# Optimization experiments

Measured on AMD Instinct MI355X. Metric: run time of the kernel, lower is better.

Reference implementation:

```python
import jax, jax.numpy as jnp
import numpy as np

K_HOPS = 3
NUM_GRAPHS = 64
GN_EPS = 1e-5


def setup_inputs() -> dict:
    key = jax.random.key(0)
    ks = jax.random.split(key, 6)
    N, E, F = 50000, 625000, 128
    y = jax.random.normal(ks[0], (N, F), dtype=jnp.float32)
    edge_index = jax.random.randint(ks[1], (2, E), 0, N, dtype=jnp.int64)
    edge_weight = jax.random.uniform(ks[2], (E,), dtype=jnp.float32)
    batch = jnp.sort(jax.random.randint(ks[3], (N,), 0, NUM_GRAPHS, dtype=jnp.int64))
    tag_w = jax.random.normal(ks[4], (K_HOPS + 1, F, F), dtype=jnp.float32) * (1.0 / np.sqrt(F))
    tag_b = jnp.zeros((F,), dtype=jnp.float32)
    gn_weight = jnp.ones((F,), dtype=jnp.float32)
    gn_bias = jnp.zeros((F,), dtype=jnp.float32)
    gn_mean_scale = jnp.ones((F,), dtype=jnp.float32)
    return {"y": y, "edge_index": edge_index, "edge_weight": edge_weight,
            "batch": batch, "tag_w": tag_w, "tag_b": tag_b,
            "gn_weight": gn_weight, "gn_bias": gn_bias, "gn_mean_scale": gn_mean_scale}


def reference(y, edge_index, edge_weight, batch, tag_w, tag_b, gn_weight, gn_bias, gn_mean_scale):
    N = y.shape[0]
    src, dst = edge_index[0], edge_index[1]

    # --- TAGConv: symmetric gcn_norm (no self-loops), K hops ---
    deg = jax.ops.segment_sum(edge_weight, dst, num_segments=N)  # [N]
    dinv = jnp.where(deg > 0, jax.lax.rsqrt(jnp.maximum(deg, 1e-30)), 0.0)
    norm = dinv[src] * edge_weight * dinv[dst]  # [E]

    h = y
    out = h @ tag_w[0]
    for k in range(1, K_HOPS + 1):
        # one hop of message passing: gather from src, scatter-sum at dst
        h = jax.ops.segment_sum(norm[:, None] * h[src], dst, num_segments=N)  # [N,F]
        out = out + h @ tag_w[k]
    out = out + tag_b

    # --- GraphNorm over per-graph segments ---
    cnt = jax.ops.segment_sum(jnp.ones((N,), out.dtype), batch, num_segments=NUM_GRAPHS)
    cnt = jnp.maximum(cnt, 1.0)[:, None]  # [G,1]
    mean = jax.ops.segment_sum(out, batch, num_segments=NUM_GRAPHS) / cnt  # [G,F]
    xc = out - gn_mean_scale * mean[batch]
    var = jax.ops.segment_sum(xc * xc, batch, num_segments=NUM_GRAPHS) / cnt  # [G,F]
    hn = gn_weight * xc * jax.lax.rsqrt(var[batch] + GN_EPS) + gn_bias

    # --- activation; dropout is identity in eval mode; residual ---
    h_act = jax.nn.relu(hn)
    return y + h_act
```

## Files before the change

kernel.cpp:

```cpp
#include <hip/hip_runtime.h>

#define F 128
#define GRAPHS 64
#define GN_EPS 1e-5f
#define SCAN_B 256
#define PB 256

typedef short short8 __attribute__((ext_vector_type(8)));
typedef float f32x4 __attribute__((ext_vector_type(4)));

__device__ __forceinline__ unsigned short f2b(float f) {
    unsigned u = __float_as_uint(f);
    unsigned r = (u + 0x7fffu + ((u >> 16) & 1u)) >> 16;
    return (unsigned short)r;
}
__device__ __forceinline__ float b2f(unsigned short h) {
    return __uint_as_float(((unsigned)h) << 16);
}

__global__ __launch_bounds__(256) void prep_kernel(const int* __restrict__ ei,
                            int* __restrict__ hist_t, int E, int NB, int chunk,
                            const float4* __restrict__ y, ushort4* __restrict__ hs0,
                            int n4, int fbl,
                            const float* __restrict__ tw, unsigned short* __restrict__ wf,
                            const int* __restrict__ batch, int* __restrict__ gstart, int n) {
    int b = blockIdx.x;
    if (b < PB) {
        __shared__ int hist[256];
        hist[threadIdx.x] = 0;
        __syncthreads();
        int e0 = b * chunk, e1 = min(e0 + chunk, E);
        for (int e = e0 + threadIdx.x; e < e1; e += 256)
            atomicAdd(&hist[ei[E + e] >> 8], 1);
        __syncthreads();
        for (int k = threadIdx.x; k < NB; k += 256)
            hist_t[k * PB + b] = hist[k];
    } else if (b < PB + fbl) {
        int i = (b - PB) * 256 + threadIdx.x;
        if (i < n4) {
            float4 v = y[i];
            hs0[i] = make_ushort4(f2b(v.x), f2b(v.y), f2b(v.z), f2b(v.w));
        }
    } else if (b < PB + fbl + 256) {
        int i = (b - PB - fbl) * 256 + threadIdx.x;
        int seg = i >> 14;
        int r = i & 16383;
        int kb = r >> 12;
        int wc = (r >> 11) & 1;
        int nt = (r >> 9) & 3;
        int lane = (r >> 3) & 63;
        int j = i & 7;
        int k = kb * 32 + (lane >> 4) * 8 + j;
        int nn = wc * 64 + nt * 16 + (lane & 15);
        wf[i] = f2b(tw[seg * 16384 + k * 128 + nn]);
    } else {
        int i = (b - PB - fbl - 256) * 256 + threadIdx.x;
        if (i < n) {
            int bb = batch[i];
            if (i == 0) {
                for (int g = 0; g <= bb; ++g) gstart[g] = 0;
            } else {
                int bp = batch[i - 1];
                for (int g = bp + 1; g <= bb; ++g) gstart[g] = i;
            }
            if (i == n - 1) {
                for (int g = bb + 1; g <= GRAPHS; ++g) gstart[g] = n;
            }
        }
    }
}

__global__ void scanA_kernel(const int* __restrict__ in, int* __restrict__ ex,
                             int* __restrict__ blockSums, int n) {
    __shared__ int s[SCAN_B];
    int i = blockIdx.x * SCAN_B + threadIdx.x;
    int v = (i < n) ? in[i] : 0;
    s[threadIdx.x] = v;
    __syncthreads();
    for (int off = 1; off < SCAN_B; off <<= 1) {
        int t = (threadIdx.x >= off) ? s[threadIdx.x - off] : 0;
        __syncthreads();
        s[threadIdx.x] += t;
        __syncthreads();
    }
    if (i < n) ex[i] = s[threadIdx.x] - v;
    if (threadIdx.x == SCAN_B - 1) blockSums[blockIdx.x] = s[SCAN_B - 1];
}

__global__ void scanB_kernel(int* __restrict__ ex, const int* __restrict__ blockSums,
                             int n, int nb) {
    __shared__ int s[SCAN_B];
    int t = threadIdx.x;
    int v = (t < nb) ? blockSums[t] : 0;
    s[t] = v;
    __syncthreads();
    for (int off = 1; off < SCAN_B; off <<= 1) {
        int x = (t >= off) ? s[t - off] : 0;
        __syncthreads();
        s[t] += x;
        __syncthreads();
    }
    int pre = (blockIdx.x == 0) ? 0 : s[blockIdx.x - 1];
    int i = blockIdx.x * SCAN_B + t;
    if (i < n) ex[i] += pre;
}

__global__ __launch_bounds__(256) void part_kernel(const int* __restrict__ ei,
                                                   const float* __restrict__ ew,
                                                   const int* __restrict__ ex,
                                                   uint2* __restrict__ part,
                                                   int E, int NB, int chunk) {
    __shared__ int cur[256];
    int k = blockIdx.x;
    for (int b = threadIdx.x; b < NB; b += 256) cur[b] = ex[b * PB + k];
    __syncthreads();
    int e0 = k * chunk, e1 = min(e0 + chunk, E);
    for (int e = e0 + threadIdx.x; e < e1; e += 256) {
        int dst = ei[E + e];
        int src = ei[e];
        float w = ew[e];
        int slot = atomicAdd(&cur[dst >> 8], 1);
        part[slot] = make_uint2(((unsigned)dst << 16) | (unsigned)src, __float_as_uint(w));
    }
}

__global__ __launch_bounds__(256) void bucket_kernel(const uint2* __restrict__ part,
                                                     const int* __restrict__ ex,
                                                     float* __restrict__ dinv,
                                                     int* __restrict__ offs,
                                                     unsigned* __restrict__ csr,
                                                     int N, int NB, int E) {
    __shared__ float degf[256];
    __shared__ int cnte[256];
    __shared__ int scn[256];
    __shared__ int cur2[256];
    int b = blockIdx.x, t = threadIdx.x;
    degf[t] = 0.f;
    cnte[t] = 0;
    __syncthreads();
    int s0 = ex[b * PB];
    int s1 = (b + 1 < NB) ? ex[(b + 1) * PB] : E;
    for (int i = s0 + t; i < s1; i += 256) {
        uint2 p = part[i];
        int dl = (p.x >> 16) & 255;
        atomicAdd(&degf[dl], __uint_as_float(p.y));
        atomicAdd(&cnte[dl], 1);
    }
    __syncthreads();
    int v = cnte[t];
    scn[t] = v;
    __syncthreads();
    for (int off = 1; off < 256; off <<= 1) {
        int x = (t >= off) ? scn[t - off] : 0;
        __syncthreads();
        scn[t] += x;
        __syncthreads();
    }
    int node = b * 256 + t;
    int base = s0 + scn[t] - v;
    if (node < N) {
        float d = degf[t];
        dinv[node] = (d > 0.f) ? rsqrtf(fmaxf(d, 1e-30f)) : 0.f;
        offs[node] = base;
    }
    if (b == 0 && t == 0) offs[N] = E;
    cur2[t] = base;
    __syncthreads();
    for (int i = s0 + t; i < s1; i += 256) {
        uint2 p = part[i];
        int dl = (p.x >> 16) & 255;
        unsigned src = p.x & 0xffffu;
        int slot = atomicAdd(&cur2[dl], 1);
        csr[slot] = (src << 16) | (unsigned)f2b(__uint_as_float(p.y));
    }
}

__global__ void wfix_kernel(unsigned* __restrict__ csr, const float* __restrict__ dinv, int E) {
    int i = blockIdx.x * 256 + threadIdx.x;
    if (i >= E) return;
    unsigned v = csr[i];
    unsigned src = v >> 16;
    float w = b2f((unsigned short)(v & 0xffffu)) * dinv[src];
    csr[i] = (src << 16) | (unsigned)f2b(w);
}

__global__ __launch_bounds__(256) void hop_kernel(const unsigned short* __restrict__ hin,
                                                  unsigned short* __restrict__ hout,
                                                  const int* __restrict__ offs,
                                                  const unsigned* __restrict__ csr,
                                                  const float* __restrict__ dinv, int n) {
    int lane = threadIdx.x & 63;
    int node = blockIdx.x * 4 + (threadIdx.x >> 6);
    if (node >= n) return;
    int g = lane >> 4, fl = lane & 15;
    int e0 = offs[node], e1 = offs[node + 1];
    float acc[8] = {};
    for (int j = e0; j < e1; j += 16) {
        int base = j + g * 4;
        int c0 = min(base + 0, e1 - 1), c1 = min(base + 1, e1 - 1);
        int c2 = min(base + 2, e1 - 1), c3 = min(base + 3, e1 - 1);
        unsigned ed0 = csr[c0], ed1 = csr[c1], ed2 = csr[c2], ed3 = csr[c3];
        float w0 = (base + 0 < e1) ? b2f((unsigned short)(ed0 & 0xffffu)) : 0.f;
        float w1 = (base + 1 < e1) ? b2f((unsigned short)(ed1 & 0xffffu)) : 0.f;
        float w2 = (base + 2 < e1) ? b2f((unsigned short)(ed2 & 0xffffu)) : 0.f;
        float w3 = (base + 3 < e1) ? b2f((unsigned short)(ed3 & 0xffffu)) : 0.f;
        short8 h0 = *(const short8*)(hin + (size_t)(ed0 >> 16) * 128 + fl * 8);
        short8 h1 = *(const short8*)(hin + (size_t)(ed1 >> 16) * 128 + fl * 8);
        short8 h2 = *(const short8*)(hin + (size_t)(ed2 >> 16) * 128 + fl * 8);
        short8 h3 = *(const short8*)(hin + (size_t)(ed3 >> 16) * 128 + fl * 8);
        #pragma unroll
        for (int k = 0; k < 8; ++k) {
            acc[k] += w0 * b2f((unsigned short)h0[k]) + w1 * b2f((unsigned short)h1[k]);
            acc[k] += w2 * b2f((unsigned short)h2[k]) + w3 * b2f((unsigned short)h3[k]);
        }
    }
    #pragma unroll
    for (int k = 0; k < 8; ++k) {
        acc[k] += __shfl_xor(acc[k], 16);
        acc[k] += __shfl_xor(acc[k], 32);
    }
    if (lane < 16) {
        float dd = dinv[node];
        short8 o;
        #pragma unroll
        for (int k = 0; k < 8; ++k) o[k] = (short)f2b(acc[k] * dd);
        *(short8*)(hout + (size_t)node * 128 + fl * 8) = o;
    }
}

__global__ __launch_bounds__(256) void gemm_kernel(const unsigned short* __restrict__ hcat,
                                                   const unsigned short* __restrict__ Wf,
                                                   const float* __restrict__ bias,
                                                   unsigned short* __restrict__ outb,
                                                   int M, size_t NF) {
    __shared__ unsigned short As[4][4096];
    int lane = threadIdx.x & 63;
    int wid = threadIdx.x >> 6;
    int wr = wid & 1, wc = wid >> 1;
    int quad = lane >> 4, l15 = lane & 15;
    int row0 = blockIdx.x * 64;
    unsigned short* myA = As[wid];
    f32x4 acc[2][4] = {};

    for (int s = 0; s < 4; ++s) {
        const unsigned short* Aseg = hcat + (size_t)s * NF;
        short8 stg[8];
        #pragma unroll
        for (int i = 0; i < 8; ++i) {
            int flat = i * 64 + lane;
            int r = flat >> 4, c = flat & 15;
            stg[i] = *(const short8*)(Aseg + (size_t)(row0 + wr * 32 + r) * 128 + c * 8);
        }
        #pragma unroll
        for (int i = 0; i < 8; ++i) {
            int flat = i * 64 + lane;
            int r = flat >> 4, c = flat & 15;
            *(short8*)&myA[(r * 16 + (c ^ (r & 15))) * 8] = stg[i];
        }
        #pragma unroll
        for (int kb = 0; kb < 4; ++kb) {
            int swz = ((kb * 4 + quad) ^ l15) * 8;
            short8 a0 = *(short8*)&myA[l15 * 128 + swz];
            short8 a1 = *(short8*)&myA[(16 + l15) * 128 + swz];
            const unsigned short* bb = Wf + (size_t)(((s * 4 + kb) * 2 + wc) * 4) * 512 + lane * 8;
            short8 b0 = *(const short8*)(bb + 0 * 512);
            short8 b1 = *(const short8*)(bb + 1 * 512);
            short8 b2 = *(const short8*)(bb + 2 * 512);
            short8 b3 = *(const short8*)(bb + 3 * 512);
            acc[0][0] = __builtin_amdgcn_mfma_f32_16x16x32_bf16(a0, b0, acc[0][0], 0, 0, 0);
            acc[0][1] = __builtin_amdgcn_mfma_f32_16x16x32_bf16(a0, b1, acc[0][1], 0, 0, 0);
            acc[0][2] = __builtin_amdgcn_mfma_f32_16x16x32_bf16(a0, b2, acc[0][2], 0, 0, 0);
            acc[0][3] = __builtin_amdgcn_mfma_f32_16x16x32_bf16(a0, b3, acc[0][3], 0, 0, 0);
            acc[1][0] = __builtin_amdgcn_mfma_f32_16x16x32_bf16(a1, b0, acc[1][0], 0, 0, 0);
            acc[1][1] = __builtin_amdgcn_mfma_f32_16x16x32_bf16(a1, b1, acc[1][1], 0, 0, 0);
            acc[1][2] = __builtin_amdgcn_mfma_f32_16x16x32_bf16(a1, b2, acc[1][2], 0, 0, 0);
            acc[1][3] = __builtin_amdgcn_mfma_f32_16x16x32_bf16(a1, b3, acc[1][3], 0, 0, 0);
        }
    }

    #pragma unroll
    for (int mt = 0; mt < 2; ++mt) {
        #pragma unroll
        for (int r = 0; r < 4; ++r) {
            int row = row0 + wr * 32 + mt * 16 + quad * 4 + r;
            if (row < M) {
                #pragma unroll
                for (int nt = 0; nt < 4; ++nt) {
                    int col = wc * 64 + nt * 16 + l15;
                    outb[(size_t)row * 128 + col] = f2b(acc[mt][nt][r] + bias[col]);
                }
            }
        }
    }
}

#define STAT_NODES 32
__global__ __launch_bounds__(256) void stats_kernel(const unsigned* __restrict__ ob2,
                                                    const int* __restrict__ batch,
                                                    float* __restrict__ S1, float* __restrict__ S2,
                                                    int n) {
    int fp = threadIdx.x & 63;
    int par = threadIdx.x >> 6;
    int base = blockIdx.x * STAT_NODES;
    int n1 = min(base + STAT_NODES, n);
    int i0 = base + par;
    if (i0 >= n1) return;
    float s1a = 0.f, s2a = 0.f, s1b = 0.f, s2b = 0.f;
    int curg = batch[i0];
    for (int i = i0; i < n1; i += 4) {
        int g = batch[i];
        if (g != curg) {
            atomicAdd(&S1[curg * F + fp * 2 + 0], s1a);
            atomicAdd(&S2[curg * F + fp * 2 + 0], s2a);
            atomicAdd(&S1[curg * F + fp * 2 + 1], s1b);
            atomicAdd(&S2[curg * F + fp * 2 + 1], s2b);
            s1a = s2a = s1b = s2b = 0.f; curg = g;
        }
        unsigned v2 = ob2[(size_t)i * 64 + fp];
        float va = b2f((unsigned short)(v2 & 0xffffu));
        float vb = b2f((unsigned short)(v2 >> 16));
        s1a += va; s2a += va * va;
        s1b += vb; s2b += vb * vb;
    }
    atomicAdd(&S1[curg * F + fp * 2 + 0], s1a);
    atomicAdd(&S2[curg * F + fp * 2 + 0], s2a);
    atomicAdd(&S1[curg * F + fp * 2 + 1], s1b);
    atomicAdd(&S2[curg * F + fp * 2 + 1], s2b);
}

__global__ void final_kernel(const ushort4* __restrict__ yb, const ushort4* __restrict__ ob,
                             const int* __restrict__ batch, const float* __restrict__ S1,
                             const float* __restrict__ S2, const int* __restrict__ gstart,
                             const float* __restrict__ gnw, const float* __restrict__ gnb,
                             const float* __restrict__ gms,
                             float4* __restrict__ res, int n) {
    int idx = blockIdx.x * blockDim.x + threadIdx.x;
    if (idx >= n * 32) return;
    int node = idx >> 5;
    int q = idx & 31;
    int g = batch[node];
    float rc = 1.f / fmaxf((float)(gstart[g + 1] - gstart[g]), 1.f);
    int base = g * 128 + q * 4;
    float4 s1 = *(const float4*)&S1[base];
    float4 s2 = *(const float4*)&S2[base];
    float4 w  = *(const float4*)&gnw[q * 4];
    float4 bb = *(const float4*)&gnb[q * 4];
    float4 sc = *(const float4*)&gms[q * 4];
    ushort4 yv = yb[idx];
    ushort4 ov = ob[idx];
    float4 r;
    {
        float m = s1.x * rc, e2 = s2.x * rc, s = sc.x;
        float var = e2 - (2.f * s - s * s) * m * m;
        float A = w.x * rsqrtf(var + GN_EPS);
        r.x = b2f(yv.x) + fmaxf(0.f, (b2f(ov.x) - s * m) * A + bb.x);
    }
    {
        float m = s1.y * rc, e2 = s2.y * rc, s = sc.y;
        float var = e2 - (2.f * s - s * s) * m * m;
        float A = w.y * rsqrtf(var + GN_EPS);
        r.y = b2f(yv.y) + fmaxf(0.f, (b2f(ov.y) - s * m) * A + bb.y);
    }
    {
        float m = s1.z * rc, e2 = s2.z * rc, s = sc.z;
        float var = e2 - (2.f * s - s * s) * m * m;
        float A = w.z * rsqrtf(var + GN_EPS);
        r.z = b2f(yv.z) + fmaxf(0.f, (b2f(ov.z) - s * m) * A + bb.z);
    }
    {
        float m = s1.w * rc, e2 = s2.w * rc, s = sc.w;
        float var = e2 - (2.f * s - s * s) * m * m;
        float A = w.w * rsqrtf(var + GN_EPS);
        r.w = b2f(yv.w) + fmaxf(0.f, (b2f(ov.w) - s * m) * A + bb.w);
    }
    res[idx] = r;
}

extern "C" void kernel_launch(void* const* d_in, const int* in_sizes, int n_in,
                              void* d_out, int out_size, void* d_ws, size_t ws_size,
                              hipStream_t stream) {
    const float* y     = (const float*)d_in[0];
    const int*   ei    = (const int*)d_in[1];
    const float* ew    = (const float*)d_in[2];
    const int*   batch = (const int*)d_in[3];
    const float* tag_w = (const float*)d_in[4];
    const float* tag_b = (const float*)d_in[5];
    const float* gnw   = (const float*)d_in[6];
    const float* gnb   = (const float*)d_in[7];
    const float* gms   = (const float*)d_in[8];
    float* res = (float*)d_out;

    const int N = in_sizes[0] / F;
    const int E = in_sizes[1] / 2;
    const size_t NF = (size_t)N * F;
    const int NB = (N + 255) >> 8;
    const int NH = NB * PB;
    const int chunk = (E + PB - 1) / PB;

    char* p = (char*)d_ws;
    float* S1 = (float*)p;       p += (size_t)GRAPHS * F * 4;
    float* S2 = (float*)p;       p += (size_t)GRAPHS * F * 4;
    size_t zeroBytes = (size_t)(p - (char*)d_ws);
    int*   gstart = (int*)p;     p += 512;
    float* dinv = (float*)p;     p += (size_t)N * 4;
    int*   offs = (int*)p;       p += (size_t)(N + 4) * 4;
    int*   hist_t = (int*)p;     p += (size_t)NH * 4;
    int*   ex = (int*)p;         p += (size_t)(NH + 4) * 4;
    int*   blockSums = (int*)p;  p += 4096;
    uint2* part = (uint2*)p;     p += (size_t)E * 8;
    unsigned* csr = (unsigned*)p; p += (size_t)E * 4;
    unsigned short* Wf = (unsigned short*)p; p += 4 * 128 * 128 * 2;
    unsigned short* hcat = (unsigned short*)p; p += NF * 2 * 4;
    unsigned short* outb = (unsigned short*)p; p += NF * 2;
    p += 4096;

    hipMemsetAsync(d_ws, 0, zeroBytes, stream);

    int n4 = N * 32;
    int fb = (n4 + 255) / 256;
    int gb = (N + 255) / 256;
    int hsb = (NH + SCAN_B - 1) / SCAN_B;

    unsigned short* hs0 = hcat;
    unsigned short* hs1 = hcat + NF;
    unsigned short* hs2 = hcat + 2 * NF;
    unsigned short* hs3 = hcat + 3 * NF;

    prep_kernel<<<PB + fb + 256 + gb, 256, 0, stream>>>(ei, hist_t, E, NB, chunk,
                                                        (const float4*)y, (ushort4*)hs0, n4, fb,
                                                        tag_w, Wf, batch, gstart, N);
    scanA_kernel<<<hsb, SCAN_B, 0, stream>>>(hist_t, ex, blockSums, NH);
    scanB_kernel<<<hsb, SCAN_B, 0, stream>>>(ex, blockSums, NH, hsb);
    part_kernel<<<PB, 256, 0, stream>>>(ei, ew, ex, part, E, NB, chunk);
    bucket_kernel<<<NB, 256, 0, stream>>>(part, ex, dinv, offs, csr, N, NB, E);
    wfix_kernel<<<(E + 255) / 256, 256, 0, stream>>>(csr, dinv, E);

    int hb = (N + 3) / 4;
    hop_kernel<<<hb, 256, 0, stream>>>(hs0, hs1, offs, csr, dinv, N);
    hop_kernel<<<hb, 256, 0, stream>>>(hs1, hs2, offs, csr, dinv, N);
    hop_kernel<<<hb, 256, 0, stream>>>(hs2, hs3, offs, csr, dinv, N);

    gemm_kernel<<<(N + 63) / 64, 256, 0, stream>>>(hcat, Wf, tag_b, outb, N, NF);

    stats_kernel<<<(N + STAT_NODES - 1) / STAT_NODES, 256, 0, stream>>>((const unsigned*)outb,
                                                                        batch, S1, S2, N);

    final_kernel<<<(N * 32 + 255) / 256, 256, 0, stream>>>((const ushort4*)hs0, (const ushort4*)outb,
                                                           batch, S1, S2, gstart, gnw, gnb, gms,
                                                           (float4*)res, N);
}
```

Measured before the change: 246.8 us.

## Fuse all stages into one cooperative persistent kernel with grid syncs

Replaces the dozen separate launches (memset, prep, two scans, partition, bucket, weight-fix, three hops, gemm, stats, final) with a single cooperative mega-kernel that loops over tasks and separates phases with grid-wide syncs. The global scan is folded into the partition phase, where each block recomputes its prefix from the histogram. The weight-fix pass is folded into the first hop, and stats is merged into the gemm phase. This removes per-launch overhead and intermediate passes, but limits parallelism to resident blocks and adds grid-sync cost. A multi-kernel fallback is kept for devices without cooperative launch.

```diff
diff --git a/kernel.cpp b/kernel.cpp
--- a/kernel.cpp
+++ b/kernel.cpp
@@ -1,9 +1,11 @@
 #include <hip/hip_runtime.h>
+#include <hip/hip_cooperative_groups.h>
+
+namespace cg = cooperative_groups;
 
 #define F 128
 #define GRAPHS 64
 #define GN_EPS 1e-5f
-#define SCAN_B 256
 #define PB 256
 
 typedef short short8 __attribute__((ext_vector_type(8)));
@@ -18,363 +20,417 @@
     return __uint_as_float(((unsigned)h) << 16);
 }
 
-__global__ __launch_bounds__(256) void prep_kernel(const int* __restrict__ ei,
-                            int* __restrict__ hist_t, int E, int NB, int chunk,
-                            const float4* __restrict__ y, ushort4* __restrict__ hs0,
-                            int n4, int fbl,
-                            const float* __restrict__ tw, unsigned short* __restrict__ wf,
-                            const int* __restrict__ batch, int* __restrict__ gstart, int n) {
-    int b = blockIdx.x;
-    if (b < PB) {
-        __shared__ int hist[256];
-        hist[threadIdx.x] = 0;
-        __syncthreads();
-        int e0 = b * chunk, e1 = min(e0 + chunk, E);
-        for (int e = e0 + threadIdx.x; e < e1; e += 256)
-            atomicAdd(&hist[ei[E + e] >> 8], 1);
-        __syncthreads();
-        for (int k = threadIdx.x; k < NB; k += 256)
-            hist_t[k * PB + b] = hist[k];
-    } else if (b < PB + fbl) {
-        int i = (b - PB) * 256 + threadIdx.x;
-        if (i < n4) {
-            float4 v = y[i];
-            hs0[i] = make_ushort4(f2b(v.x), f2b(v.y), f2b(v.z), f2b(v.w));
-        }
-    } else if (b < PB + fbl + 256) {
-        int i = (b - PB - fbl) * 256 + threadIdx.x;
-        int seg = i >> 14;
-        int r = i & 16383;
-        int kb = r >> 12;
-        int wc = (r >> 11) & 1;
-        int nt = (r >> 9) & 3;
-        int lane = (r >> 3) & 63;
-        int j = i & 7;
-        int k = kb * 32 + (lane >> 4) * 8 + j;
-        int nn = wc * 64 + nt * 16 + (lane & 15);
-        wf[i] = f2b(tw[seg * 16384 + k * 128 + nn]);
-    } else {
-        int i = (b - PB - fbl - 256) * 256 + threadIdx.x;
-        if (i < n) {
-            int bb = batch[i];
-            if (i == 0) {
-                for (int g = 0; g <= bb; ++g) gstart[g] = 0;
-            } else {
-                int bp = batch[i - 1];
-                for (int g = bp + 1; g <= bb; ++g) gstart[g] = i;
-            }
-            if (i == n - 1) {
-                for (int g = bb + 1; g <= GRAPHS; ++g) gstart[g] = n;
-            }
-        }
-    }
-}
-
-__global__ void scanA_kernel(const int* __restrict__ in, int* __restrict__ ex,
-                             int* __restrict__ blockSums, int n) {
-    __shared__ int s[SCAN_B];
-    int i = blockIdx.x * SCAN_B + threadIdx.x;
-    int v = (i < n) ? in[i] : 0;
-    s[threadIdx.x] = v;
-    __syncthreads();
-    for (int off = 1; off < SCAN_B; off <<= 1) {
-        int t = (threadIdx.x >= off) ? s[threadIdx.x - off] : 0;
-        __syncthreads();
-        s[threadIdx.x] += t;
-        __syncthreads();
-    }
-    if (i < n) ex[i] = s[threadIdx.x] - v;
-    if (threadIdx.x == SCAN_B - 1) blockSums[blockIdx.x] = s[SCAN_B - 1];
-}
-
-__global__ void scanB_kernel(int* __restrict__ ex, const int* __restrict__ blockSums,
-                             int n, int nb) {
-    __shared__ int s[SCAN_B];
+struct MArgs {
+    const float* y; const int* ei; const float* ew; const int* batch;
+    const float* tw; const float* tb; const float* gnw; const float* gnb; const float* gms;
+    float* res;
+    float* S1; float* S2; int* gstart; float* dinv; int* offs; int* hist_t; int* bbase;
+    uint2* part; unsigned* csr; unsigned short* Wf; unsigned short* hcat; unsigned short* outb;
+    int N, E, NB, chunk, fb, gb;
+    size_t NF;
+};
+
+__device__ void ph_prep(const MArgs& a, char* smem) {
+    int* hist = (int*)smem;
+    const int t0 = 256;
+    const int t1 = t0 + a.fb;
+    const int t2 = t1 + 256;
+    const int t3 = t2 + a.gb;
+    const int t4 = t3 + 8;
+    int tid = threadIdx.x;
+    for (int task = blockIdx.x; task < t4; task += gridDim.x) {
+        if (task < t0) {
+            __syncthreads();
+            hist[tid] = 0;
+            __syncthreads();
+            int e0 = task * a.chunk, e1 = min(e0 + a.chunk, a.E);
+            for (int e = e0 + tid; e < e1; e += 256)
+                atomicAdd(&hist[a.ei[a.E + e] >> 8], 1);
+            __syncthreads();
+            for (int k = tid; k < a.NB; k += 256)
+                a.hist_t[k * PB + task] = hist[k];
+        } else if (task < t1) {
+            int i = (task - t0) * 256 + tid;
+            if (i < a.N * 32) {
+                float4 v = ((const float4*)a.y)[i];
+                ((ushort4*)a.hcat)[i] = make_ushort4(f2b(v.x), f2b(v.y), f2b(v.z), f2b(v.w));
+            }
+        } else if (task < t2) {
+            int i = (task - t1) * 256 + tid;
+            int seg = i >> 14;
+            int r = i & 16383;
+            int kb = r >> 12;
+            int wcc = (r >> 11) & 1;
+            int ntt = (r >> 9) & 3;
+            int lane = (r >> 3) & 63;
+            int j = i & 7;
+            int k = kb * 32 + (lane >> 4) * 8 + j;
+            int nn = wcc * 64 + ntt * 16 + (lane & 15);
+            a.Wf[i] = f2b(a.tw[seg * 16384 + k * 128 + nn]);
+        } else if (task < t3) {
+            int i = (task - t2) * 256 + tid;
+            if (i < a.N) {
+                int bb = a.batch[i];
+                if (i == 0) {
+                    for (int g = 0; g <= bb; ++g) a.gstart[g] = 0;
+                } else {
+                    int bp = a.batch[i - 1];
+                    for (int g = bp + 1; g <= bb; ++g) a.gstart[g] = i;
+                }
+                if (i == a.N - 1) {
+                    for (int g = bb + 1; g <= GRAPHS; ++g) a.gstart[g] = a.N;
+                }
+            }
+        } else {
+            int z = task - t3;
+            float* dst = a.S1 + z * 2048;
+            for (int i2 = tid; i2 < 2048; i2 += 256) dst[i2] = 0.f;
+        }
+    }
+}
+
+__device__ void ph_part(const MArgs& a, char* smem) {
+    int* cur = (int*)smem;
+    int* rs  = cur + 256;
     int t = threadIdx.x;
-    int v = (t < nb) ? blockSums[t] : 0;
-    s[t] = v;
-    __syncthreads();
-    for (int off = 1; off < SCAN_B; off <<= 1) {
-        int x = (t >= off) ? s[t - off] : 0;
-        __syncthreads();
-        s[t] += x;
-        __syncthreads();
-    }
-    int pre = (blockIdx.x == 0) ? 0 : s[blockIdx.x - 1];
-    int i = blockIdx.x * SCAN_B + t;
-    if (i < n) ex[i] += pre;
-}
-
-__global__ __launch_bounds__(256) void part_kernel(const int* __restrict__ ei,
-                                                   const float* __restrict__ ew,
-                                                   const int* __restrict__ ex,
-                                                   uint2* __restrict__ part,
-                                                   int E, int NB, int chunk) {
-    __shared__ int cur[256];
-    int k = blockIdx.x;
-    for (int b = threadIdx.x; b < NB; b += 256) cur[b] = ex[b * PB + k];
-    __syncthreads();
-    int e0 = k * chunk, e1 = min(e0 + chunk, E);
-    for (int e = e0 + threadIdx.x; e < e1; e += 256) {
-        int dst = ei[E + e];
-        int src = ei[e];
-        float w = ew[e];
-        int slot = atomicAdd(&cur[dst >> 8], 1);
-        part[slot] = make_uint2(((unsigned)dst << 16) | (unsigned)src, __float_as_uint(w));
-    }
-}
-
-__global__ __launch_bounds__(256) void bucket_kernel(const uint2* __restrict__ part,
-                                                     const int* __restrict__ ex,
-                                                     float* __restrict__ dinv,
-                                                     int* __restrict__ offs,
-                                                     unsigned* __restrict__ csr,
-                                                     int N, int NB, int E) {
-    __shared__ float degf[256];
-    __shared__ int cnte[256];
-    __shared__ int scn[256];
-    __shared__ int cur2[256];
-    int b = blockIdx.x, t = threadIdx.x;
-    degf[t] = 0.f;
-    cnte[t] = 0;
-    __syncthreads();
-    int s0 = ex[b * PB];
-    int s1 = (b + 1 < NB) ? ex[(b + 1) * PB] : E;
-    for (int i = s0 + t; i < s1; i += 256) {
-        uint2 p = part[i];
-        int dl = (p.x >> 16) & 255;
-        atomicAdd(&degf[dl], __uint_as_float(p.y));
-        atomicAdd(&cnte[dl], 1);
-    }
-    __syncthreads();
-    int v = cnte[t];
-    scn[t] = v;
-    __syncthreads();
-    for (int off = 1; off < 256; off <<= 1) {
-        int x = (t >= off) ? scn[t - off] : 0;
-        __syncthreads();
-        scn[t] += x;
-        __syncthreads();
-    }
-    int node = b * 256 + t;
-    int base = s0 + scn[t] - v;
-    if (node < N) {
-        float d = degf[t];
-        dinv[node] = (d > 0.f) ? rsqrtf(fmaxf(d, 1e-30f)) : 0.f;
-        offs[node] = base;
-    }
-    if (b == 0 && t == 0) offs[N] = E;
-    cur2[t] = base;
-    __syncthreads();
-    for (int i = s0 + t; i < s1; i += 256) {
-        uint2 p = part[i];
-        int dl = (p.x >> 16) & 255;
-        unsigned src = p.x & 0xffffu;
-        int slot = atomicAdd(&cur2[dl], 1);
-        csr[slot] = (src << 16) | (unsigned)f2b(__uint_as_float(p.y));
-    }
-}
-
-__global__ void wfix_kernel(unsigned* __restrict__ csr, const float* __restrict__ dinv, int E) {
-    int i = blockIdx.x * 256 + threadIdx.x;
-    if (i >= E) return;
-    unsigned v = csr[i];
-    unsigned src = v >> 16;
-    float w = b2f((unsigned short)(v & 0xffffu)) * dinv[src];
-    csr[i] = (src << 16) | (unsigned)f2b(w);
-}
-
-__global__ __launch_bounds__(256) void hop_kernel(const unsigned short* __restrict__ hin,
-                                                  unsigned short* __restrict__ hout,
-                                                  const int* __restrict__ offs,
-                                                  const unsigned* __restrict__ csr,
-                                                  const float* __restrict__ dinv, int n) {
+    for (int k = blockIdx.x; k < PB; k += gridDim.x) {
+        __syncthreads();
+        int total = 0, pref = 0;
+        if (t < a.NB) {
+            const int4* row = (const int4*)(a.hist_t + t * PB);
+            for (int q = 0; q < PB / 4; ++q) {
+                int4 v = row[q];
+                int c4 = q * 4;
+                total += v.x + v.y + v.z + v.w;
+                if (c4 + 4 <= k) pref += v.x + v.y + v.z + v.w;
+                else {
+                    if (c4 + 0 < k) pref += v.x;
+                    if (c4 + 1 < k) pref += v.y;
+                    if (c4 + 2 < k) pref += v.z;
+                    if (c4 + 3 < k) pref += v.w;
+                }
+            }
+        }
+        rs[t] = (t < a.NB) ? total : 0;
+        __syncthreads();
+        for (int off = 1; off < 256; off <<= 1) {
+            int x = (t >= off) ? rs[t - off] : 0;
+            __syncthreads();
+            rs[t] += x;
+            __syncthreads();
+        }
+        int rowStart = (t > 0) ? rs[t - 1] : 0;
+        cur[t] = rowStart + pref;
+        if (k == 0 && t <= a.NB) a.bbase[t] = rowStart;
+        __syncthreads();
+        int e0 = k * a.chunk, e1 = min(e0 + a.chunk, a.E);
+        for (int e = e0 + t; e < e1; e += 256) {
+            int dst = a.ei[a.E + e];
+            int src = a.ei[e];
+            float w = a.ew[e];
+            int slot = atomicAdd(&cur[dst >> 8], 1);
+            a.part[slot] = make_uint2(((unsigned)dst << 16) | (unsigned)src, __float_as_uint(w));
+        }
+    }
+}
+
+__device__ void ph_bucket(const MArgs& a, char* smem) {
+    float* degf = (float*)smem;
+    int* cnte = (int*)(smem + 1024);
+    int* scn  = (int*)(smem + 2048);
+    int* cur2 = (int*)(smem + 3072);
+    int t = threadIdx.x;
+    for (int b = blockIdx.x; b < a.NB; b += gridDim.x) {
+        __syncthreads();
+        degf[t] = 0.f;
+        cnte[t] = 0;
+        __syncthreads();
+        int s0 = a.bbase[b];
+        int s1 = a.bbase[b + 1];
+        for (int i = s0 + t; i < s1; i += 256) {
+            uint2 pp = a.part[i];
+            int dl = (pp.x >> 16) & 255;
+            atomicAdd(&degf[dl], __uint_as_float(pp.y));
+            atomicAdd(&cnte[dl], 1);
+        }
+        __syncthreads();
+        int v = cnte[t];
+        scn[t] = v;
+        __syncthreads();
+        for (int off = 1; off < 256; off <<= 1) {
+            int x = (t >= off) ? scn[t - off] : 0;
+            __syncthreads();
+            scn[t] += x;
+            __syncthreads();
+        }
+        int node = b * 256 + t;
+        int base = s0 + scn[t] - v;
+        if (node < a.N) {
+            float d = degf[t];
+            a.dinv[node] = (d > 0.f) ? rsqrtf(fmaxf(d, 1e-30f)) : 0.f;
+            a.offs[node] = base;
+        }
+        if (b == 0 && t == 0) a.offs[a.N] = a.E;
+        cur2[t] = base;
+        __syncthreads();
+        for (int i = s0 + t; i < s1; i += 256) {
+            uint2 pp = a.part[i];
+            int dl = (pp.x >> 16) & 255;
+            unsigned src = pp.x & 0xffffu;
+            int slot = atomicAdd(&cur2[dl], 1);
+            a.csr[slot] = (src << 16) | (unsigned)f2b(__uint_as_float(pp.y));
+        }
+    }
+}
+
+template<bool FIX>
+__device__ void ph_hop(const MArgs& a, const unsigned short* __restrict__ hin,
+                       unsigned short* __restrict__ hout) {
     int lane = threadIdx.x & 63;
-    int node = blockIdx.x * 4 + (threadIdx.x >> 6);
-    if (node >= n) return;
-    int g = lane >> 4, fl = lane & 15;
-    int e0 = offs[node], e1 = offs[node + 1];
-    float acc[8] = {};
-    for (int j = e0; j < e1; j += 16) {
-        int base = j + g * 4;
-        int c0 = min(base + 0, e1 - 1), c1 = min(base + 1, e1 - 1);
-        int c2 = min(base + 2, e1 - 1), c3 = min(base + 3, e1 - 1);
-        unsigned ed0 = csr[c0], ed1 = csr[c1], ed2 = csr[c2], ed3 = csr[c3];
-        float w0 = (base + 0 < e1) ? b2f((unsigned short)(ed0 & 0xffffu)) : 0.f;
-        float w1 = (base + 1 < e1) ? b2f((unsigned short)(ed1 & 0xffffu)) : 0.f;
-        float w2 = (base + 2 < e1) ? b2f((unsigned short)(ed2 & 0xffffu)) : 0.f;
-        float w3 = (base + 3 < e1) ? b2f((unsigned short)(ed3 & 0xffffu)) : 0.f;
-        short8 h0 = *(const short8*)(hin + (size_t)(ed0 >> 16) * 128 + fl * 8);
-        short8 h1 = *(const short8*)(hin + (size_t)(ed1 >> 16) * 128 + fl * 8);
-        short8 h2 = *(const short8*)(hin + (size_t)(ed2 >> 16) * 128 + fl * 8);
-        short8 h3 = *(const short8*)(hin + (size_t)(ed3 >> 16) * 128 + fl * 8);
+    int wv = threadIdx.x >> 6;
+    int gq = lane >> 4, fl = lane & 15;
+    int hb = (a.N + 3) >> 2;
+    for (int task = blockIdx.x; task < hb; task += gridDim.x) {
+        int node = task * 4 + wv;
+        if (node >= a.N) continue;
+        int e0 = a.offs[node], e1 = a.offs[node + 1];
+        float acc[8] = {};
+        for (int j = e0; j < e1; j += 16) {
+            int base = j + gq * 4;
+            int c0 = min(base + 0, e1 - 1), c1 = min(base + 1, e1 - 1);
+            int c2 = min(base + 2, e1 - 1), c3 = min(base + 3, e1 - 1);
+            unsigned ed0 = a.csr[c0], ed1 = a.csr[c1], ed2 = a.csr[c2], ed3 = a.csr[c3];
+            float w0 = (base + 0 < e1) ? b2f((unsigned short)(ed0 & 0xffffu)) : 0.f;
+            float w1 = (base + 1 < e1) ? b2f((unsigned short)(ed1 & 0xffffu)) : 0.f;
+            float w2 = (base + 2 < e1) ? b2f((unsigned short)(ed2 & 0xffffu)) : 0.f;
+            float w3 = (base + 3 < e1) ? b2f((unsigned short)(ed3 & 0xffffu)) : 0.f;
+            if (FIX) {
+                w0 *= a.dinv[ed0 >> 16];
+                w1 *= a.dinv[ed1 >> 16];
+                w2 *= a.dinv[ed2 >> 16];
+                w3 *= a.dinv[ed3 >> 16];
+            }
+            short8 h0 = *(const short8*)(hin + (size_t)(ed0 >> 16) * 128 + fl * 8);
+            short8 h1 = *(const short8*)(hin + (size_t)(ed1 >> 16) * 128 + fl * 8);
+            short8 h2 = *(const short8*)(hin + (size_t)(ed2 >> 16) * 128 + fl * 8);
+            short8 h3 = *(const short8*)(hin + (size_t)(ed3 >> 16) * 128 + fl * 8);
+            if (FIX && fl < 4) {
+                int wi = base + fl;
+                if (wi < e1) {
+                    float wf2 = (fl == 0) ? w0 : (fl == 1) ? w1 : (fl == 2) ? w2 : w3;
+                    unsigned ede = (fl == 0) ? ed0 : (fl == 1) ? ed1 : (fl == 2) ? ed2 : ed3;
+                    a.csr[wi] = (ede & 0xffff0000u) | (unsigned)f2b(wf2);
+                }
+            }
+            #pragma unroll
+            for (int k = 0; k < 8; ++k) {
+                acc[k] += w0 * b2f((unsigned short)h0[k]) + w1 * b2f((unsigned short)h1[k]);
+                acc[k] += w2 * b2f((unsigned short)h2[k]) + w3 * b2f((unsigned short)h3[k]);
+            }
+        }
         #pragma unroll
         for (int k = 0; k < 8; ++k) {
-            acc[k] += w0 * b2f((unsigned short)h0[k]) + w1 * b2f((unsigned short)h1[k]);
-            acc[k] += w2 * b2f((unsigned short)h2[k]) + w3 * b2f((unsigned short)h3[k]);
-        }
-    }
-    #pragma unroll
-    for (int k = 0; k < 8; ++k) {
-        acc[k] += __shfl_xor(acc[k], 16);
-        acc[k] += __shfl_xor(acc[k], 32);
-    }
-    if (lane < 16) {
-        float dd = dinv[node];
-        short8 o;
-        #pragma unroll
-        for (int k = 0; k < 8; ++k) o[k] = (short)f2b(acc[k] * dd);
-        *(short8*)(hout + (size_t)node * 128 + fl * 8) = o;
-    }
-}
-
-__global__ __launch_bounds__(256) void gemm_kernel(const unsigned short* __restrict__ hcat,
-                                                   const unsigned short* __restrict__ Wf,
-                                                   const float* __restrict__ bias,
-                                                   unsigned short* __restrict__ outb,
-                                                   int M, size_t NF) {
-    __shared__ unsigned short As[4][4096];
+            acc[k] += __shfl_xor(acc[k], 16);
+            acc[k] += __shfl_xor(acc[k], 32);
+        }
+        if (lane < 16) {
+            float dd = a.dinv[node];
+            short8 o;
+            #pragma unroll
+            for (int k = 0; k < 8; ++k) o[k] = (short)f2b(acc[k] * dd);
+            *(short8*)(hout + (size_t)node * 128 + fl * 8) = o;
+        }
+    }
+}
+
+__device__ void ph_gemm(const MArgs& a, char* smem) {
+    unsigned short (*As)[4096] = (unsigned short (*)[4096])smem;
+    const unsigned short* __restrict__ hcat = a.hcat;
+    const unsigned short* __restrict__ Wf = a.Wf;
+    const float* bias = a.tb;
+    int M = a.N;
+    size_t NF = a.NF;
     int lane = threadIdx.x & 63;
     int wid = threadIdx.x >> 6;
     int wr = wid & 1, wc = wid >> 1;
     int quad = lane >> 4, l15 = lane & 15;
-    int row0 = blockIdx.x * 64;
-    unsigned short* myA = As[wid];
-    f32x4 acc[2][4] = {};
-
-    for (int s = 0; s < 4; ++s) {
-        const unsigned short* Aseg = hcat + (size_t)s * NF;
-        short8 stg[8];
+    int ntiles = (M + 63) >> 6;
+    for (int task = blockIdx.x; task < ntiles; task += gridDim.x) {
+        int row0 = task * 64;
+        f32x4 acc[2][4] = {};
+        for (int s = 0; s < 4; ++s) {
+            const unsigned short* Aseg = hcat + (size_t)s * NF;
+            short8 stg[4];
+            #pragma unroll
+            for (int i = 0; i < 4; ++i) {
+                int flat = (wc * 4 + i) * 64 + lane;
+                int r = flat >> 4, c = flat & 15;
+                stg[i] = *(const short8*)(Aseg + (size_t)(row0 + wr * 32 + r) * 128 + c * 8);
+            }
+            __syncthreads();
+            #pragma unroll
+            for (int i = 0; i < 4; ++i) {
+                int flat = (wc * 4 + i) * 64 + lane;
+                int r = flat >> 4, c = flat & 15;
+                *(short8*)&As[wr][(r * 16 + (c ^ (r & 15))) * 8] = stg[i];
+            }
+            __syncthreads();
+            #pragma unroll
+            for (int kb = 0; kb < 4; ++kb) {
+                int swz = ((kb * 4 + quad) ^ l15) * 8;
+                short8 a0 = *(short8*)&As[wr][l15 * 128 + swz];
+                short8 a1 = *(short8*)&As[wr][(16 + l15) * 128 + swz];
+                const unsigned short* bb = Wf + (size_t)(((s * 4 + kb) * 2 + wc) * 4) * 512 + lane * 8;
+                short8 b0 = *(const short8*)(bb + 0 * 512);
+                short8 b1 = *(const short8*)(bb + 1 * 512);
+                short8 b2 = *(const short8*)(bb + 2 * 512);
+                short8 b3 = *(const short8*)(bb + 3 * 512);
+                acc[0][0] = __builtin_amdgcn_mfma_f32_16x16x32_bf16(a0, b0, acc[0][0], 0, 0, 0);
+                acc[0][1] = __builtin_amdgcn_mfma_f32_16x16x32_bf16(a0, b1, acc[0][1], 0, 0, 0);
+                acc[0][2] = __builtin_amdgcn_mfma_f32_16x16x32_bf16(a0, b2, acc[0][2], 0, 0, 0);
+                acc[0][3] = __builtin_amdgcn_mfma_f32_16x16x32_bf16(a0, b3, acc[0][3], 0, 0, 0);
+                acc[1][0] = __builtin_amdgcn_mfma_f32_16x16x32_bf16(a1, b0, acc[1][0], 0, 0, 0);
+                acc[1][1] = __builtin_amdgcn_mfma_f32_16x16x32_bf16(a1, b1, acc[1][1], 0, 0, 0);
+                acc[1][2] = __builtin_amdgcn_mfma_f32_16x16x32_bf16(a1, b2, acc[1][2], 0, 0, 0);
+                acc[1][3] = __builtin_amdgcn_mfma_f32_16x16x32_bf16(a1, b3, acc[1][3], 0, 0, 0);
+            }
+        }
+
+        float bcol[4];
         #pragma unroll
-        for (int i = 0; i < 8; ++i) {
-            int flat = i * 64 + lane;
-            int r = flat >> 4, c = flat & 15;
-            stg[i] = *(const short8*)(Aseg + (size_t)(row0 + wr * 32 + r) * 128 + c * 8);
-        }
+        for (int nt = 0; nt < 4; ++nt) bcol[nt] = bias[wc * 64 + nt * 16 + l15];
+        int rg[2][4];
         #pragma unroll
-        for (int i = 0; i < 8; ++i) {
-            int flat = i * 64 + lane;
-            int r = flat >> 4, c = flat & 15;
-            *(short8*)&myA[(r * 16 + (c ^ (r & 15))) * 8] = stg[i];
-        }
-        #pragma unroll
-        for (int kb = 0; kb < 4; ++kb) {
-            int swz = ((kb * 4 + quad) ^ l15) * 8;
-            short8 a0 = *(short8*)&myA[l15 * 128 + swz];
-            short8 a1 = *(short8*)&myA[(16 + l15) * 128 + swz];
-            const unsigned short* bb = Wf + (size_t)(((s * 4 + kb) * 2 + wc) * 4) * 512 + lane * 8;
-            short8 b0 = *(const short8*)(bb + 0 * 512);
-            short8 b1 = *(const short8*)(bb + 1 * 512);
-            short8 b2 = *(const short8*)(bb + 2 * 512);
-            short8 b3 = *(const short8*)(bb + 3 * 512);
-            acc[0][0] = __builtin_amdgcn_mfma_f32_16x16x32_bf16(a0, b0, acc[0][0], 0, 0, 0);
-            acc[0][1] = __builtin_amdgcn_mfma_f32_16x16x32_bf16(a0, b1, acc[0][1], 0, 0, 0);
-            acc[0][2] = __builtin_amdgcn_mfma_f32_16x16x32_bf16(a0, b2, acc[0][2], 0, 0, 0);
-            acc[0][3] = __builtin_amdgcn_mfma_f32_16x16x32_bf16(a0, b3, acc[0][3], 0, 0, 0);
-            acc[1][0] = __builtin_amdgcn_mfma_f32_16x16x32_bf16(a1, b0, acc[1][0], 0, 0, 0);
-            acc[1][1] = __builtin_amdgcn_mfma_f32_16x16x32_bf16(a1, b1, acc[1][1], 0, 0, 0);
-            acc[1][2] = __builtin_amdgcn_mfma_f32_16x16x32_bf16(a1, b2, acc[1][2], 0, 0, 0);
-            acc[1][3] = __builtin_amdgcn_mfma_f32_16x16x32_bf16(a1, b3, acc[1][3], 0, 0, 0);
-        }
-    }
-
-    #pragma unroll
-    for (int mt = 0; mt < 2; ++mt) {
-        #pragma unroll
-        for (int r = 0; r < 4; ++r) {
-            int row = row0 + wr * 32 + mt * 16 + quad * 4 + r;
-            if (row < M) {
+        for (int mt = 0; mt < 2; ++mt) {
+            #pragma unroll
+            for (int r = 0; r < 4; ++r) {
+                int row = row0 + wr * 32 + mt * 16 + quad * 4 + r;
+                rg[mt][r] = (row < M) ? a.batch[row] : -1;
+                if (row < M) {
+                    #pragma unroll
+                    for (int nt = 0; nt < 4; ++nt) {
+                        float vv = acc[mt][nt][r] + bcol[nt];
+                        a.outb[(size_t)row * 128 + wc * 64 + nt * 16 + l15] = f2b(vv);
+                    }
+                }
+            }
+        }
+        int glo = a.batch[row0];
+        int ghi = a.batch[min(row0 + 63, M - 1)];
+        for (int g = glo; g <= ghi; ++g) {
+            float s1[4] = {0.f, 0.f, 0.f, 0.f}, s2[4] = {0.f, 0.f, 0.f, 0.f};
+            #pragma unroll
+            for (int mt = 0; mt < 2; ++mt) {
+                #pragma unroll
+                for (int r = 0; r < 4; ++r) {
+                    if (rg[mt][r] == g) {
+                        #pragma unroll
+                        for (int nt = 0; nt < 4; ++nt) {
+                            float vv = acc[mt][nt][r] + bcol[nt];
+                            s1[nt] += vv;
+                            s2[nt] += vv * vv;
+                        }
+                    }
+                }
+            }
+            #pragma unroll
+            for (int nt = 0; nt < 4; ++nt) {
+                s1[nt] += __shfl_xor(s1[nt], 16);
+                s1[nt] += __shfl_xor(s1[nt], 32);
+                s2[nt] += __shfl_xor(s2[nt], 16);
+                s2[nt] += __shfl_xor(s2[nt], 32);
+            }
+            if (quad == 0) {
                 #pragma unroll
                 for (int nt = 0; nt < 4; ++nt) {
                     int col = wc * 64 + nt * 16 + l15;
-                    outb[(size_t)row * 128 + col] = f2b(acc[mt][nt][r] + bias[col]);
-                }
-            }
-        }
-    }
-}
-
-#define STAT_NODES 32
-__global__ __launch_bounds__(256) void stats_kernel(const unsigned* __restrict__ ob2,
-                                                    const int* __restrict__ batch,
-                                                    float* __restrict__ S1, float* __restrict__ S2,
-                                                    int n) {
-    int fp = threadIdx.x & 63;
-    int par = threadIdx.x >> 6;
-    int base = blockIdx.x * STAT_NODES;
-    int n1 = min(base + STAT_NODES, n);
-    int i0 = base + par;
-    if (i0 >= n1) return;
-    float s1a = 0.f, s2a = 0.f, s1b = 0.f, s2b = 0.f;
-    int curg = batch[i0];
-    for (int i = i0; i < n1; i += 4) {
-        int g = batch[i];
-        if (g != curg) {
-            atomicAdd(&S1[curg * F + fp * 2 + 0], s1a);
-            atomicAdd(&S2[curg * F + fp * 2 + 0], s2a);
-            atomicAdd(&S1[curg * F + fp * 2 + 1], s1b);
-            atomicAdd(&S2[curg * F + fp * 2 + 1], s2b);
-            s1a = s2a = s1b = s2b = 0.f; curg = g;
-        }
-        unsigned v2 = ob2[(size_t)i * 64 + fp];
-        float va = b2f((unsigned short)(v2 & 0xffffu));
-        float vb = b2f((unsigned short)(v2 >> 16));
-        s1a += va; s2a += va * va;
-        s1b += vb; s2b += vb * vb;
-    }
-    atomicAdd(&S1[curg * F + fp * 2 + 0], s1a);
-    atomicAdd(&S2[curg * F + fp * 2 + 0], s2a);
-    atomicAdd(&S1[curg * F + fp * 2 + 1], s1b);
-    atomicAdd(&S2[curg * F + fp * 2 + 1], s2b);
-}
-
-__global__ void final_kernel(const ushort4* __restrict__ yb, const ushort4* __restrict__ ob,
-                             const int* __restrict__ batch, const float* __restrict__ S1,
-                             const float* __restrict__ S2, const int* __restrict__ gstart,
-                             const float* __restrict__ gnw, const float* __restrict__ gnb,
-                             const float* __restrict__ gms,
-                             float4* __restrict__ res, int n) {
-    int idx = blockIdx.x * blockDim.x + threadIdx.x;
-    if (idx >= n * 32) return;
-    int node = idx >> 5;
-    int q = idx & 31;
-    int g = batch[node];
-    float rc = 1.f / fmaxf((float)(gstart[g + 1] - gstart[g]), 1.f);
-    int base = g * 128 + q * 4;
-    float4 s1 = *(const float4*)&S1[base];
-    float4 s2 = *(const float4*)&S2[base];
-    float4 w  = *(const float4*)&gnw[q * 4];
-    float4 bb = *(const float4*)&gnb[q * 4];
-    float4 sc = *(const float4*)&gms[q * 4];
-    ushort4 yv = yb[idx];
-    ushort4 ov = ob[idx];
-    float4 r;
-    {
-        float m = s1.x * rc, e2 = s2.x * rc, s = sc.x;
-        float var = e2 - (2.f * s - s * s) * m * m;
-        float A = w.x * rsqrtf(var + GN_EPS);
-        r.x = b2f(yv.x) + fmaxf(0.f, (b2f(ov.x) - s * m) * A + bb.x);
-    }
-    {
-        float m = s1.y * rc, e2 = s2.y * rc, s = sc.y;
-        float var = e2 - (2.f * s - s * s) * m * m;
-        float A = w.y * rsqrtf(var + GN_EPS);
-        r.y = b2f(yv.y) + fmaxf(0.f, (b2f(ov.y) - s * m) * A + bb.y);
-    }
-    {
-        float m = s1.z * rc, e2 = s2.z * rc, s = sc.z;
-        float var = e2 - (2.f * s - s * s) * m * m;
-        float A = w.z * rsqrtf(var + GN_EPS);
-        r.z = b2f(yv.z) + fmaxf(0.f, (b2f(ov.z) - s * m) * A + bb.z);
-    }
-    {
-        float m = s1.w * rc, e2 = s2.w * rc, s = sc.w;
-        float var = e2 - (2.f * s - s * s) * m * m;
-        float A = w.w * rsqrtf(var + GN_EPS);
-        r.w = b2f(yv.w) + fmaxf(0.f, (b2f(ov.w) - s * m) * A + bb.w);
-    }
-    res[idx] = r;
-}
+                    atomicAdd(&a.S1[g * 128 + col], s1[nt]);
+                    atomicAdd(&a.S2[g * 128 + col], s2[nt]);
+                }
+            }
+        }
+    }
+}
+
+__device__ void ph_final(const MArgs& a) {
+    int total = a.N * 32;
+    const ushort4* yb = (const ushort4*)a.hcat;
+    const ushort4* ob = (const ushort4*)a.outb;
+    float4* res = (float4*)a.res;
+    for (int idx = blockIdx.x * 256 + threadIdx.x; idx < total; idx += gridDim.x * 256) {
+        int node = idx >> 5;
+        int q = idx & 31;
+        int g = a.batch[node];
+        float rc = 1.f / fmaxf((float)(a.gstart[g + 1] - a.gstart[g]), 1.f);
+        int base = g * 128 + q * 4;
+        float4 s1 = *(const float4*)&a.S1[base];
+        float4 s2 = *(const float4*)&a.S2[base];
+        float4 w  = *(const float4*)&a.gnw[q * 4];
+        float4 bb = *(const float4*)&a.gnb[q * 4];
+        float4 sc = *(const float4*)&a.gms[q * 4];
+        ushort4 yv = yb[idx];
+        ushort4 ov = ob[idx];
+        float4 r;
+        {
+            float m = s1.x * rc, e2 = s2.x * rc, s = sc.x;
+            float var = e2 - (2.f * s - s * s) * m * m;
+            float A = w.x * rsqrtf(var + GN_EPS);
+            r.x = b2f(yv.x) + fmaxf(0.f, (b2f(ov.x) - s * m) * A + bb.x);
+        }
+        {
+            float m = s1.y * rc, e2 = s2.y * rc, s = sc.y;
+            float var = e2 - (2.f * s - s * s) * m * m;
+            float A = w.y * rsqrtf(var + GN_EPS);
+            r.y = b2f(yv.y) + fmaxf(0.f, (b2f(ov.y) - s * m) * A + bb.y);
+        }
+        {
+            float m = s1.z * rc, e2 = s2.z * rc, s = sc.z;
+            float var = e2 - (2.f * s - s * s) * m * m;
+            float A = w.z * rsqrtf(var + GN_EPS);
+            r.z = b2f(yv.z) + fmaxf(0.f, (b2f(ov.z) - s * m) * A + bb.z);
+        }
+        {
+            float m = s1.w * rc, e2 = s2.w * rc, s = sc.w;
+            float var = e2 - (2.f * s - s * s) * m * m;
+            float A = w.w * rsqrtf(var + GN_EPS);
+            r.w = b2f(yv.w) + fmaxf(0.f, (b2f(ov.w) - s * m) * A + bb.w);
+        }
+        res[idx] = r;
+    }
+}
+
+__global__ __launch_bounds__(256, 2) void mega_kernel(MArgs a) {
+    __shared__ __align__(16) char smem[16384];
+    cg::grid_group grid = cg::this_grid();
+    ph_prep(a, smem);
+    grid.sync();
+    ph_part(a, smem);
+    grid.sync();
+    ph_bucket(a, smem);
+    grid.sync();
+    ph_hop<true>(a, a.hcat, a.hcat + a.NF);
+    grid.sync();
+    ph_hop<false>(a, a.hcat + a.NF, a.hcat + 2 * a.NF);
+    grid.sync();
+    ph_hop<false>(a, a.hcat + 2 * a.NF, a.hcat + 3 * a.NF);
+    grid.sync();
+    ph_gemm(a, smem);
+    grid.sync();
+    ph_final(a);
+}
+
+__global__ __launch_bounds__(256) void k_prep(MArgs a)   { __shared__ __align__(16) char sm[1024];  ph_prep(a, sm); }
+__global__ __launch_bounds__(256) void k_part(MArgs a)   { __shared__ __align__(16) char sm[2048];  ph_part(a, sm); }
+__global__ __launch_bounds__(256) void k_bucket(MArgs a) { __shared__ __align__(16) char sm[4096];  ph_bucket(a, sm); }
+template<int H>
+__global__ __launch_bounds__(256) void k_hop(MArgs a) {
+    const unsigned short* hin = a.hcat + (size_t)(H - 1) * a.NF;
+    unsigned short* hout = a.hcat + (size_t)H * a.NF;
+    if constexpr (H == 1) ph_hop<true>(a, hin, hout);
+    else ph_hop<false>(a, hin, hout);
+}
+__global__ __launch_bounds__(256) void k_gemm(MArgs a)   { __shared__ __align__(16) char sm[16384]; ph_gemm(a, sm); }
+__global__ __launch_bounds__(256) void k_final(MArgs a)  { ph_final(a); }
 
 extern "C" void kernel_launch(void* const* d_in, const int* in_sizes, int n_in,
                               void* d_out, int out_size, void* d_ws, size_t ws_size,
@@ -388,7 +444,6 @@
     const float* gnw   = (const float*)d_in[6];
     const float* gnb   = (const float*)d_in[7];
     const float* gms   = (const float*)d_in[8];
-    float* res = (float*)d_out;
 
     const int N = in_sizes[0] / F;
     const int E = in_sizes[1] / 2;
@@ -396,17 +451,17 @@
     const int NB = (N + 255) >> 8;
     const int NH = NB * PB;
     const int chunk = (E + PB - 1) / PB;
+    const int fb = (N * 32 + 255) / 256;
+    const int gb = (N + 255) / 256;
 
     char* p = (char*)d_ws;
     float* S1 = (float*)p;       p += (size_t)GRAPHS * F * 4;
     float* S2 = (float*)p;       p += (size_t)GRAPHS * F * 4;
-    size_t zeroBytes = (size_t)(p - (char*)d_ws);
     int*   gstart = (int*)p;     p += 512;
     float* dinv = (float*)p;     p += (size_t)N * 4;
     int*   offs = (int*)p;       p += (size_t)(N + 4) * 4;
     int*   hist_t = (int*)p;     p += (size_t)NH * 4;
-    int*   ex = (int*)p;         p += (size_t)(NH + 4) * 4;
-    int*   blockSums = (int*)p;  p += 4096;
+    int*   bbase = (int*)p;      p += 1040;
     uint2* part = (uint2*)p;     p += (size_t)E * 8;
     unsigned* csr = (unsigned*)p; p += (size_t)E * 4;
     unsigned short* Wf = (unsigned short*)p; p += 4 * 128 * 128 * 2;
@@ -414,38 +469,47 @@
     unsigned short* outb = (unsigned short*)p; p += NF * 2;
     p += 4096;
 
-    hipMemsetAsync(d_ws, 0, zeroBytes, stream);
-
-    int n4 = N * 32;
-    int fb = (n4 + 255) / 256;
-    int gb = (N + 255) / 256;
-    int hsb = (NH + SCAN_B - 1) / SCAN_B;
-
-    unsigned short* hs0 = hcat;
-    unsigned short* hs1 = hcat + NF;
-    unsigned short* hs2 = hcat + 2 * NF;
-    unsigned short* hs3 = hcat + 3 * NF;
-
-    prep_kernel<<<PB + fb + 256 + gb, 256, 0, stream>>>(ei, hist_t, E, NB, chunk,
-                                                        (const float4*)y, (ushort4*)hs0, n4, fb,
-                                                        tag_w, Wf, batch, gstart, N);
-    scanA_kernel<<<hsb, SCAN_B, 0, stream>>>(hist_t, ex, blockSums, NH);
-    scanB_kernel<<<hsb, SCAN_B, 0, stream>>>(ex, blockSums, NH, hsb);
-    part_kernel<<<PB, 256, 0, stream>>>(ei, ew, ex, part, E, NB, chunk);
-    bucket_kernel<<<NB, 256, 0, stream>>>(part, ex, dinv, offs, csr, N, NB, E);
-    wfix_kernel<<<(E + 255) / 256, 256, 0, stream>>>(csr, dinv, E);
-
-    int hb = (N + 3) / 4;
-    hop_kernel<<<hb, 256, 0, stream>>>(hs0, hs1, offs, csr, dinv, N);
-    hop_kernel<<<hb, 256, 0, stream>>>(hs1, hs2, offs, csr, dinv, N);
-    hop_kernel<<<hb, 256, 0, stream>>>(hs2, hs3, offs, csr, dinv, N);
-
-    gemm_kernel<<<(N + 63) / 64, 256, 0, stream>>>(hcat, Wf, tag_b, outb, N, NF);
-
-    stats_kernel<<<(N + STAT_NODES - 1) / STAT_NODES, 256, 0, stream>>>((const unsigned*)outb,
-                                                                        batch, S1, S2, N);
-
-    final_kernel<<<(N * 32 + 255) / 256, 256, 0, stream>>>((const ushort4*)hs0, (const ushort4*)outb,
-                                                           batch, S1, S2, gstart, gnw, gnb, gms,
-                                                           (float4*)res, N);
-}
+    MArgs ha;
+    ha.y = y; ha.ei = ei; ha.ew = ew; ha.batch = batch;
+    ha.tw = tag_w; ha.tb = tag_b; ha.gnw = gnw; ha.gnb = gnb; ha.gms = gms;
+    ha.res = (float*)d_out;
+    ha.S1 = S1; ha.S2 = S2; ha.gstart = gstart; ha.dinv = dinv; ha.offs = offs;
+    ha.hist_t = hist_t; ha.bbase = bbase; ha.part = part; ha.csr = csr;
+    ha.Wf = Wf; ha.hcat = hcat; ha.outb = outb;
+    ha.N = N; ha.E = E; ha.NB = NB; ha.chunk = chunk; ha.fb = fb; ha.gb = gb;
+    ha.NF = NF;
+
+    static int coop = -1;
+    static int nblk = 512;
+    if (coop < 0) {
+        int dev = 0;
+        hipGetDevice(&dev);
+        int sup = 0;
+        hipDeviceGetAttribute(&sup, hipDeviceAttributeCooperativeLaunch, dev);
+        hipDeviceProp_t prop;
+        hipGetDeviceProperties(&prop, dev);
+        int mb = 0;
+        hipOccupancyMaxActiveBlocksPerMultiprocessor(&mb, (const void*)mega_kernel, 256, 0);
+        if (mb < 1) mb = 1;
+        nblk = prop.multiProcessorCount * mb;
+        coop = sup ? 1 : 0;
+    }
+
+    if (coop) {
+        void* params[] = { (void*)&ha };
+        hipError_t err = hipLaunchCooperativeKernel((const void*)mega_kernel,
+                                                    dim3(nblk), dim3(256),
+                                                    params, 0, stream);
+        if (err == hipSuccess) return;
+        coop = 0;
+    }
+
+    k_prep<<<256 + fb + 256 + gb + 8, 256, 0, stream>>>(ha);
+    k_part<<<PB, 256, 0, stream>>>(ha);
+    k_bucket<<<NB, 256, 0, stream>>>(ha);
+    k_hop<1><<<(N + 3) / 4, 256, 0, stream>>>(ha);
+    k_hop<2><<<(N + 3) / 4, 256, 0, stream>>>(ha);
+    k_hop<3><<<(N + 3) / 4, 256, 0, stream>>>(ha);
+    k_gemm<<<(N + 63) / 64, 256, 0, stream>>>(ha);
+    k_final<<<(N * 32 + 255) / 256, 256, 0, stream>>>(ha);
+}
```

New measurement: 719.4 us. +191.5%, slower.
